# Performance work log

Hardware: AMD Instinct MI355X
Metric: run time of the kernel (lower is better)

## Reference

```python
import jax, jax.numpy as jnp
import numpy as np

# db4 decomposition filters (pywt convention)
DB4_LO = np.array([-0.010597401784997278, 0.032883011666982945, 0.030841381835986965,
                   -0.18703481171888114, -0.02798376941698385, 0.6308807679295904,
                   0.7148465705525415, 0.23037781330885523], dtype=np.float32)
DB4_HI = np.array([-0.23037781330885523, 0.7148465705525415, -0.6308807679295904,
                   -0.02798376941698385, 0.18703481171888114, 0.030841381835986965,
                   -0.032883011666982945, -0.010597401784997278], dtype=np.float32)
PAD = 3


def setup_inputs() -> dict:
    key = jax.random.key(0)
    x = jax.random.normal(key, (4, 3, 32, 256, 256), dtype=jnp.float32)
    filt = jnp.stack([jnp.asarray(DB4_LO), jnp.asarray(DB4_HI)])  # [2, 8]
    return {"x": x, "filt": filt}


def _dwt1d(x, filt, axis):
    """Analysis filter bank along one axis: reflect-pad, true convolution
    with (dec_lo, dec_hi), stride 2. Returns (low, high) with that axis halved."""
    x = jnp.moveaxis(x, axis, -1)
    shp = x.shape
    L = shp[-1]
    x2 = x.reshape(-1, 1, L)
    x2 = jnp.pad(x2, ((0, 0), (0, 0), (PAD, PAD)), mode="reflect")
    # flip filters so lax correlation == mathematical convolution with dec filters
    k = jnp.flip(filt, axis=-1)[:, None, :]  # [2, 1, 8]
    y = jax.lax.conv_general_dilated(
        x2, k, window_strides=(2,), padding="VALID",
        dimension_numbers=("NCH", "OIH", "NCH"))  # [N, 2, L//2]
    y = y.reshape(shp[:-1] + (2, L // 2))
    lo = jnp.moveaxis(y[..., 0, :], -1, axis)
    hi = jnp.moveaxis(y[..., 1, :], -1, axis)
    return lo, hi


def reference(x, filt):
    # x: [B, C, T, H, W] -> [B, 8C, T/2, H/2, W/2]
    lo_t, hi_t = _dwt1d(x, filt, 2)
    subbands = []
    for a in (lo_t, hi_t):
        lo_h, hi_h = _dwt1d(a, filt, 3)
        for b in (lo_h, hi_h):
            lo_w, hi_w = _dwt1d(b, filt, 4)
            subbands.append(lo_w)
            subbands.append(hi_w)
    # order: LLL, LLH, LHL, LHH, HLL, HLH, HHL, HHH (t,h,w)
    return jnp.concatenate(subbands, axis=1)
```

## Files before the change

### kernel.cpp

```cpp
#include <hip/hip_runtime.h>
#include <hip/hip_bf16.h>


#define CC 3
#define TT 32
#define HH 256
#define WW 256
#define TOH 16
#define HOH 128
#define WOH 128

#define TH 4
#define TW 32
#define NROWS 14
#define ROWW 70
#define RSLOT 128
#define NSLOTS 8
#define DEPTH 6
#define NW 8
#define NTHREADS 512
#define VSTR 512
#define NRR (4*NROWS)

constexpr float GLO[8] = {
     0.23037781330885523f,  0.7148465705525415f,   0.6308807679295904f,
    -0.02798376941698385f, -0.18703481171888114f,  0.030841381835986965f,
     0.032883011666982945f, -0.010597401784997278f };
constexpr float GHI[8] = {
    -0.010597401784997278f, -0.032883011666982945f, 0.030841381835986965f,
     0.18703481171888114f,  -0.02798376941698385f,  -0.6308807679295904f,
     0.7148465705525415f,   -0.23037781330885523f };

__device__ __forceinline__ int refl(int p, int n) {
    p = p < 0 ? -p : p;
    p = p >= n ? 2 * n - 2 - p : p;
    return p;
}

__global__ __launch_bounds__(NTHREADS)
void dwt3d_db4_kernel(const float* __restrict__ x, float* __restrict__ out) {
    __shared__ float Ring[NW * NSLOTS * RSLOT];
    __shared__ __hip_bfloat16 Vbuf[TT * VSTR];

    const int tid  = threadIdx.x;
    const int wid  = tid >> 6;
    const int lane = tid & 63;
    const int wo   = lane & 31;
    const int sw   = lane >> 5;

    const int lin = blockIdx.x;
    const int nid = (lin & 7) * 192 + (lin >> 3);
    const int wo0 = (nid & 3) * TW;
    const int ho0 = ((nid >> 2) & 31) * TH;
    const int bz  = nid >> 7;
    const int b = bz / CC, c = bz - b * CC;

    const float* xs = x + (size_t)bz * (TT * HH * WW);

    const int gcol0 = refl(2 * wo0 - 3 + lane, WW);
    const int l6    = lane < 6 ? lane : 5;
    const int gcol1 = refl(2 * wo0 - 3 + 64 + l6, WW);

    float wG[8];
#pragma unroll
    for (int j = 0; j < 8; ++j) wG[j] = sw ? GHI[j] : GLO[j];

    const int t0 = wid * 4;
    const int ringbase = wid * (NSLOTS * RSLOT);

#define ISSUE(rr_) do {                                                       \
        const int t_ = (rr_) / NROWS, r_ = (rr_) % NROWS;                     \
        const int gr_ = refl(2 * ho0 - 3 + r_, HH);                           \
        const float* rowp_ = xs + (size_t)(t0 + t_) * (HH * WW) + gr_ * WW;   \
        float* lp_ = &Ring[ringbase + ((rr_) & (NSLOTS - 1)) * RSLOT];        \
        __builtin_amdgcn_global_load_lds(                                     \
            (const __attribute__((address_space(1))) void*)(rowp_ + gcol0),   \
            (__attribute__((address_space(3))) void*)lp_, 4, 0, 0);           \
        __builtin_amdgcn_global_load_lds(                                     \
            (const __attribute__((address_space(1))) void*)(rowp_ + gcol1),   \
            (__attribute__((address_space(3))) void*)(lp_ + 64), 4, 0, 0);    \
    } while (0)

    float vacc[8] = {0.f, 0.f, 0.f, 0.f, 0.f, 0.f, 0.f, 0.f};

#pragma unroll
    for (int rr = 0; rr < DEPTH; ++rr) ISSUE(rr);

#pragma unroll
    for (int rr = 0; rr < NRR; ++rr) {
        {
            const int vm = (NRR - 1 - rr) * 2 < 10 ? (NRR - 1 - rr) * 2 : 10;
            if      (vm >= 10) asm volatile("s_waitcnt vmcnt(10)" ::: "memory");
            else if (vm == 8)  asm volatile("s_waitcnt vmcnt(8)"  ::: "memory");
            else if (vm == 6)  asm volatile("s_waitcnt vmcnt(6)"  ::: "memory");
            else if (vm == 4)  asm volatile("s_waitcnt vmcnt(4)"  ::: "memory");
            else if (vm == 2)  asm volatile("s_waitcnt vmcnt(2)"  ::: "memory");
            else               asm volatile("s_waitcnt vmcnt(0)"  ::: "memory");
        }

        const int rbase = ringbase + (rr & (NSLOTS - 1)) * RSLOT + 2 * wo;
        float m = 0.f;
#pragma unroll
        for (int j = 0; j < 8; ++j) m = fmaf(Ring[rbase + j], wG[j], m);

        if (rr + DEPTH < NRR) ISSUE(rr + DEPTH);

        const int r = rr % NROWS;
#pragma unroll
        for (int ho = 0; ho < 4; ++ho) {
            const int j = r - 2 * ho;
            if (j >= 0 && j < 8) {
                vacc[ho]     = fmaf(m, GLO[j], vacc[ho]);
                vacc[4 + ho] = fmaf(m, GHI[j], vacc[4 + ho]);
            }
        }

        if (r == NROWS - 1) {
            const int t = t0 + rr / NROWS;
#pragma unroll
            for (int sh = 0; sh < 2; ++sh)
#pragma unroll
                for (int ho = 0; ho < 4; ++ho)
                    Vbuf[t * VSTR + (2 * sh + sw) * 128 + ho * 32 + wo] =
                        __float2bfloat16(vacc[sh * 4 + ho]);
#pragma unroll
            for (int q = 0; q < 8; ++q) vacc[q] = 0.f;
        }
    }

    __syncthreads();

    float v[TT];
#pragma unroll
    for (int t = 0; t < TT; ++t) v[t] = __bfloat162float(Vbuf[t * VSTR + tid]);

    const int subhw = tid >> 7;
    const int hoq   = (tid >> 5) & 3;
    const int wo2   = tid & 31;

    const size_t hw = (size_t)(ho0 + hoq) * WOH + (wo0 + wo2);
    const size_t ch_lo = (size_t)(subhw * CC + c);
    const size_t ch_hi = (size_t)((4 + subhw) * CC + c);
    const size_t o_lo = (((size_t)b * 24 + ch_lo) * TOH) * (HOH * WOH) + hw;
    const size_t o_hi = (((size_t)b * 24 + ch_hi) * TOH) * (HOH * WOH) + hw;

#pragma unroll
    for (int to = 0; to < TOH; ++to) {
        float lo = 0.f, hi = 0.f;
#pragma unroll
        for (int j = 0; j < 8; ++j) {
            int p = 2 * to + j - 3;
            p = p < 0 ? -p : p;
            p = p >= TT ? 2 * TT - 2 - p : p;
            lo = fmaf(v[p], GLO[j], lo);
            hi = fmaf(v[p], GHI[j], hi);
        }
        out[o_lo + (size_t)to * (HOH * WOH)] = lo;
        out[o_hi + (size_t)to * (HOH * WOH)] = hi;
    }
}

extern "C" void kernel_launch(void* const* d_in, const int* in_sizes, int n_in,
                              void* d_out, int out_size, void* d_ws, size_t ws_size,
                              hipStream_t stream) {
    (void)in_sizes; (void)n_in; (void)d_ws; (void)ws_size; (void)out_size;
    const float* x = (const float*)d_in[0];
    float* out = (float*)d_out;
    dim3 grid(1536, 1, 1);
    dim3 block(NTHREADS);
    hipLaunchKernelGGL(dwt3d_db4_kernel, grid, block, 0, stream, x, out);
}
```

Baseline: 46.87 us.

## Split rows across half-waves with float2 LDS reads and shuffle-reduced H accumulation

Each half-wave now handles alternate input rows (even/odd) of a row pair and computes both the low and high W-filter outputs from float2 LDS loads, instead of each half computing one of lo/hi for every row. Each iteration processes two rows and issues two prefetches, and the vmcnt waits are adjusted to match. The H-filter taps are split by parity, and the partial sums from the two halves are combined with a cross-half shuffle before the bf16 store. This is meant to cut scalar LDS reads and loop overhead, at the cost of more accumulator registers and an extra shuffle.

```diff
diff --git a/kernel.cpp b/kernel.cpp
--- a/kernel.cpp
+++ b/kernel.cpp
@@ -13,14 +13,15 @@
 #define TH 4
 #define TW 32
 #define NROWS 14
-#define ROWW 70
 #define RSLOT 128
+#define RSLOT2 64
 #define NSLOTS 8
 #define DEPTH 6
 #define NW 8
 #define NTHREADS 512
 #define VSTR 512
 #define NRR (4*NROWS)
+#define NIT (NRR/2)
 
 constexpr float GLO[8] = {
      0.23037781330885523f,  0.7148465705525415f,   0.6308807679295904f,
@@ -46,7 +47,7 @@
     const int wid  = tid >> 6;
     const int lane = tid & 63;
     const int wo   = lane & 31;
-    const int sw   = lane >> 5;
+    const int p    = lane >> 5;
 
     const int lin = blockIdx.x;
     const int nid = (lin & 7) * 192 + (lin >> 3);
@@ -61,12 +62,18 @@
     const int l6    = lane < 6 ? lane : 5;
     const int gcol1 = refl(2 * wo0 - 3 + 64 + l6, WW);
 
-    float wG[8];
+    float wH0[4], wH1[4];
 #pragma unroll
-    for (int j = 0; j < 8; ++j) wG[j] = sw ? GHI[j] : GLO[j];
+    for (int d = 0; d < 4; ++d) {
+        wH0[d] = p ? GLO[2 * d + 1] : GLO[2 * d];
+        wH1[d] = p ? GHI[2 * d + 1] : GHI[2 * d];
+    }
 
     const int t0 = wid * 4;
     const int ringbase = wid * (NSLOTS * RSLOT);
+    const float2* Ring2 = (const float2*)Ring;
+    const int r2base = wid * (NSLOTS * RSLOT2) + p * RSLOT2 + wo;
+    const int vcolbase = p * 128 + wo;
 
 #define ISSUE(rr_) do {                                                       \
         const int t_ = (rr_) / NROWS, r_ = (rr_) % NROWS;                     \
@@ -81,50 +88,68 @@
             (__attribute__((address_space(3))) void*)(lp_ + 64), 4, 0, 0);    \
     } while (0)
 
-    float vacc[8] = {0.f, 0.f, 0.f, 0.f, 0.f, 0.f, 0.f, 0.f};
+    float vacc0[2][4], vacc1[2][4];
+#pragma unroll
+    for (int sh = 0; sh < 2; ++sh)
+#pragma unroll
+        for (int ho = 0; ho < 4; ++ho) { vacc0[sh][ho] = 0.f; vacc1[sh][ho] = 0.f; }
 
 #pragma unroll
     for (int rr = 0; rr < DEPTH; ++rr) ISSUE(rr);
 
 #pragma unroll
-    for (int rr = 0; rr < NRR; ++rr) {
+    for (int k = 0; k < NIT; ++k) {
+        if (k <= 25)      asm volatile("s_waitcnt vmcnt(8)" ::: "memory");
+        else if (k == 26) asm volatile("s_waitcnt vmcnt(4)" ::: "memory");
+        else              asm volatile("s_waitcnt vmcnt(0)" ::: "memory");
+
+        const int soff = ((2 * k) & (NSLOTS - 1)) * RSLOT2;
+        const float2 d0 = Ring2[r2base + soff + 0];
+        const float2 d1 = Ring2[r2base + soff + 1];
+        const float2 d2 = Ring2[r2base + soff + 2];
+        const float2 d3 = Ring2[r2base + soff + 3];
+
+        float m_lo, m_hi;
         {
-            const int vm = (NRR - 1 - rr) * 2 < 10 ? (NRR - 1 - rr) * 2 : 10;
-            if      (vm >= 10) asm volatile("s_waitcnt vmcnt(10)" ::: "memory");
-            else if (vm == 8)  asm volatile("s_waitcnt vmcnt(8)"  ::: "memory");
-            else if (vm == 6)  asm volatile("s_waitcnt vmcnt(6)"  ::: "memory");
-            else if (vm == 4)  asm volatile("s_waitcnt vmcnt(4)"  ::: "memory");
-            else if (vm == 2)  asm volatile("s_waitcnt vmcnt(2)"  ::: "memory");
-            else               asm volatile("s_waitcnt vmcnt(0)"  ::: "memory");
+            float a0 = d0.x, a1 = d0.y, a2 = d1.x, a3 = d1.y;
+            float a4 = d2.x, a5 = d2.y, a6 = d3.x, a7 = d3.y;
+            m_lo = a0 * GLO[0]; m_hi = a0 * GHI[0];
+            m_lo = fmaf(a1, GLO[1], m_lo); m_hi = fmaf(a1, GHI[1], m_hi);
+            m_lo = fmaf(a2, GLO[2], m_lo); m_hi = fmaf(a2, GHI[2], m_hi);
+            m_lo = fmaf(a3, GLO[3], m_lo); m_hi = fmaf(a3, GHI[3], m_hi);
+            m_lo = fmaf(a4, GLO[4], m_lo); m_hi = fmaf(a4, GHI[4], m_hi);
+            m_lo = fmaf(a5, GLO[5], m_lo); m_hi = fmaf(a5, GHI[5], m_hi);
+            m_lo = fmaf(a6, GLO[6], m_lo); m_hi = fmaf(a6, GHI[6], m_hi);
+            m_lo = fmaf(a7, GLO[7], m_lo); m_hi = fmaf(a7, GHI[7], m_hi);
         }
 
-        const int rbase = ringbase + (rr & (NSLOTS - 1)) * RSLOT + 2 * wo;
-        float m = 0.f;
-#pragma unroll
-        for (int j = 0; j < 8; ++j) m = fmaf(Ring[rbase + j], wG[j], m);
+        if (2 * k + 6 < NRR) { ISSUE(2 * k + 6); ISSUE(2 * k + 7); }
 
-        if (rr + DEPTH < NRR) ISSUE(rr + DEPTH);
-
-        const int r = rr % NROWS;
+        const int kk = k % 7;
 #pragma unroll
         for (int ho = 0; ho < 4; ++ho) {
-            const int j = r - 2 * ho;
-            if (j >= 0 && j < 8) {
-                vacc[ho]     = fmaf(m, GLO[j], vacc[ho]);
-                vacc[4 + ho] = fmaf(m, GHI[j], vacc[4 + ho]);
+            const int d = kk - ho;
+            if (d >= 0 && d < 4) {
+                vacc0[0][ho] = fmaf(m_lo, wH0[d], vacc0[0][ho]);
+                vacc0[1][ho] = fmaf(m_lo, wH1[d], vacc0[1][ho]);
+                vacc1[0][ho] = fmaf(m_hi, wH0[d], vacc1[0][ho]);
+                vacc1[1][ho] = fmaf(m_hi, wH1[d], vacc1[1][ho]);
             }
         }
 
-        if (r == NROWS - 1) {
-            const int t = t0 + rr / NROWS;
+        if (kk == 6) {
+            const int t = t0 + k / 7;
 #pragma unroll
             for (int sh = 0; sh < 2; ++sh)
 #pragma unroll
-                for (int ho = 0; ho < 4; ++ho)
-                    Vbuf[t * VSTR + (2 * sh + sw) * 128 + ho * 32 + wo] =
-                        __float2bfloat16(vacc[sh * 4 + ho]);
-#pragma unroll
-            for (int q = 0; q < 8; ++q) vacc[q] = 0.f;
+                for (int ho = 0; ho < 4; ++ho) {
+                    const float send = p ? vacc0[sh][ho] : vacc1[sh][ho];
+                    const float keep = p ? vacc1[sh][ho] : vacc0[sh][ho];
+                    const float recv = __shfl_xor(send, 32, 64);
+                    Vbuf[t * VSTR + sh * 256 + vcolbase + ho * 32] =
+                        __float2bfloat16(keep + recv);
+                    vacc0[sh][ho] = 0.f; vacc1[sh][ho] = 0.f;
+                }
         }
     }
 
@@ -149,11 +174,11 @@
         float lo = 0.f, hi = 0.f;
 #pragma unroll
         for (int j = 0; j < 8; ++j) {
-            int p = 2 * to + j - 3;
-            p = p < 0 ? -p : p;
-            p = p >= TT ? 2 * TT - 2 - p : p;
-            lo = fmaf(v[p], GLO[j], lo);
-            hi = fmaf(v[p], GHI[j], hi);
+            int q = 2 * to + j - 3;
+            q = q < 0 ? -q : q;
+            q = q >= TT ? 2 * TT - 2 - q : q;
+            lo = fmaf(v[q], GLO[j], lo);
+            hi = fmaf(v[q], GHI[j], hi);
         }
         out[o_lo + (size_t)to * (HOH * WOH)] = lo;
         out[o_hi + (size_t)to * (HOH * WOH)] = hi;
```

After: 46.00 us. No clear change (-1.9%).
